# Optimization experiments

Measured on AMD Instinct MI355X. Metric: run time of the kernel, lower is better.

Reference implementation:

```python
import jax, jax.numpy as jnp
import numpy as np

H = 4  # head_num
K_CONV = 1  # convolution_num


def mhsa_mean(x, Wq, Wk, Wv, Wo):
    # x: [..., L, d]; standard multi-head self-attention followed by mean over L
    d = x.shape[-1]
    hd = d // H
    q = (x @ Wq).reshape(x.shape[:-1] + (H, hd))
    k = (x @ Wk).reshape(x.shape[:-1] + (H, hd))
    v = (x @ Wv).reshape(x.shape[:-1] + (H, hd))
    scores = jnp.einsum('...lhd,...mhd->...hlm', q, k) / jnp.sqrt(jnp.asarray(hd, x.dtype))
    attn = jax.nn.softmax(scores, axis=-1)
    o = jnp.einsum('...hlm,...mhd->...lhd', attn, v).reshape(x.shape) @ Wo
    return o.mean(axis=-2)


def setup_inputs() -> dict:
    key = jax.random.key(0)
    ks = jax.random.split(key, 18)
    WORD, QUERY, ENT, REV = 50000, 50000, 100000, 100000
    DW, DE = 64, 64
    LQ, LR, E, B = 8, 8, 2000000, 1024
    W_word = jax.random.normal(ks[0], (WORD, DW), jnp.float32) * 0.02
    W_word = W_word.at[0].set(0.0)  # padding_idx=0
    W_query = jax.random.normal(ks[1], (QUERY, DE), jnp.float32) * 0.02
    W_entity = jax.random.normal(ks[2], (ENT, DE), jnp.float32) * 0.02
    Wq = jax.random.normal(ks[3], (DW, DW), jnp.float32) * 0.05
    Wk = jax.random.normal(ks[4], (DW, DW), jnp.float32) * 0.05
    Wv = jax.random.normal(ks[5], (DW, DW), jnp.float32) * 0.05
    Wo = jax.random.normal(ks[6], (DW, DW), jnp.float32) * 0.05
    query_word_ids = jax.random.randint(ks[7], (QUERY, LQ), 0, WORD)
    review_word_ids = jax.random.randint(ks[8], (REV, LR), 0, WORD)
    profile_dst = jax.random.randint(ks[9], (REV,), 0, ENT)
    p_src = jax.random.randint(ks[10], (E,), 0, ENT)
    p_dst = jax.random.randint(ks[11], (E,), 0, ENT)
    p_qid = jax.random.randint(ks[12], (E,), 0, QUERY)
    users = jax.random.randint(ks[13], (B,), 0, ENT)
    items = jax.random.randint(ks[14], (B,), 0, ENT)
    negs = jax.random.randint(ks[15], (B,), 0, ENT)
    query_words = jax.random.randint(ks[16], (B, LQ), 0, WORD)
    return {'W_word': W_word, 'W_query': W_query, 'W_entity': W_entity,
            'Wq': Wq, 'Wk': Wk, 'Wv': Wv, 'Wo': Wo,
            'query_word_ids': query_word_ids, 'review_word_ids': review_word_ids,
            'profile_dst': profile_dst, 'p_src': p_src, 'p_dst': p_dst, 'p_qid': p_qid,
            'users': users, 'items': items, 'negs': negs, 'query_words': query_words}


def reference(W_word, W_query, W_entity, Wq, Wk, Wv, Wo,
              query_word_ids, review_word_ids, profile_dst, p_src, p_dst, p_qid,
              users, items, negs, query_words):
    N = W_entity.shape[0]
    DE = W_query.shape[1]
    # --- doc embeddings via MHSA+mean over composing words ---
    h_query = mhsa_mean(W_word[query_word_ids], Wq, Wk, Wv, Wo)    # [Q, DW]
    h_review = mhsa_mean(W_word[review_word_ids], Wq, Wk, Wv, Wo)  # [R, DW]
    # --- profiles: sum reviews into entities, degree-normalize ---
    deg_p = jnp.maximum(jax.ops.segment_sum(jnp.ones(profile_dst.shape[0], jnp.float32), profile_dst, num_segments=N), 1.0)
    ent_h = jax.ops.segment_sum(h_review, profile_dst, num_segments=N) / deg_p[:, None]
    q_e0 = jnp.concatenate([W_query, h_query], axis=-1)   # [Q, D]
    e_k = jnp.concatenate([W_entity, ent_h], axis=-1)     # e_0 [N, D]
    # --- interaction degrees: out-deg(purchased) + out-deg(purchased_by) ---
    ones_e = jnp.ones(p_src.shape[0], jnp.float32)
    deg_i = jax.ops.segment_sum(ones_e, p_src, num_segments=N) + jax.ops.segment_sum(ones_e, p_dst, num_segments=N)
    inv_sqrt = 1.0 / jnp.sqrt(jnp.maximum(deg_i, 1.0))    # [N]
    q_edge = q_e0[p_qid]                                   # [E, D]
    e_acc = e_k
    for _ in range(K_CONV):
        # purchased: m = src.e_k + q_e0[q_id] / sqrt(deg_i[src]); sum to dst
        msg = e_k[p_src] + q_edge * inv_sqrt[p_src][:, None]
        agg = jax.ops.segment_sum(msg, p_dst, num_segments=N)
        # purchased_by (reverse edges): m = e_k[src]/sqrt(deg_i[src]); sum to dst
        agg = agg + jax.ops.segment_sum(e_k[p_dst] * inv_sqrt[p_dst][:, None], p_src, num_segments=N)
        e_k = agg * inv_sqrt[:, None]
        e_acc = e_acc + e_k
    e = e_acc / (K_CONV + 1)                               # [N, D]
    # --- batch forward (train mode) ---
    qb = mhsa_mean(W_word[query_words], Wq, Wk, Wv, Wo)    # [B, DW]
    qb = jnp.concatenate([jnp.zeros((qb.shape[0], DE), qb.dtype), qb], axis=-1)
    personalized = e[users] + qb
    return personalized, e[items], e[negs]
```

## Files before the change

kernel.cpp:

```cpp
#include <hip/hip_runtime.h>

typedef unsigned int uint;
typedef unsigned short ushort;

typedef __bf16 bf16x8 __attribute__((ext_vector_type(8)));
typedef float f32x4 __attribute__((ext_vector_type(4)));
union U8 { uint4 u4; uint w[4]; bf16x8 b; };

__device__ __forceinline__ float bf2f(ushort u) {
    return __uint_as_float(((uint)u) << 16);
}
__device__ __forceinline__ float2 bfp2f(uint u) {
    float2 r;
    r.x = __uint_as_float(u << 16);
    r.y = __uint_as_float(u & 0xffff0000u);
    return r;
}
__device__ __forceinline__ ushort f2bf(float f) {
    uint u = __float_as_uint(f);
    return (ushort)((u + 0x7fffu + ((u >> 16) & 1u)) >> 16);
}

__global__ void mark_kernel(const int* __restrict__ users,
                            const int* __restrict__ items,
                            const int* __restrict__ negs,
                            int* __restrict__ mapid, int* __restrict__ mcnt,
                            int B) {
    int t = blockIdx.x * blockDim.x + threadIdx.x;
    if (t >= 3 * B) return;
    int n = t < B ? users[t] : (t < 2 * B ? items[t - B] : negs[t - 2 * B]);
    int old = atomicCAS(&mapid[n], -1, -2);
    if (old == -1) mapid[n] = atomicAdd(mcnt, 1);
}

__global__ void pre_kernel(const float* __restrict__ W_word,
                           const float* __restrict__ Wq,
                           const float* __restrict__ Wk,
                           const float* __restrict__ Wv,
                           const float* __restrict__ Wo,
                           ushort* __restrict__ Pq, ushort* __restrict__ Pk,
                           ushort* __restrict__ Vt,
                           const float* __restrict__ W_query,
                           const float* __restrict__ W_entity,
                           ushort* __restrict__ qe0b, ushort* __restrict__ e0b,
                           const int* __restrict__ p_src,
                           const int* __restrict__ p_dst,
                           const int* __restrict__ profile_dst,
                           const int* __restrict__ mapid,
                           int* __restrict__ degc, int* __restrict__ degp,
                           int* __restrict__ deg2,
                           int WORD, int Qn, int N, int E, int R,
                           int nc_blk, int npj_blk, int ncq_blk, int nce_blk) {
    int bid = blockIdx.x;
    int g = bid >> 3, j = bid & 7;
    if ((g & 3) == 3) {
        int idx = (g >> 2) * 8 + j;
        if (idx >= nc_blk) return;
        int t = idx * 256 + threadIdx.x;
        if (t < E) {
            int s = p_src[t], d = p_dst[t];
            atomicAdd(&degc[s], 1);
            atomicAdd(&degc[d], 1);
            int md = mapid[d]; if (md >= 0) atomicAdd(&deg2[md], 1);
            int ms = mapid[s]; if (ms >= 0) atomicAdd(&deg2[ms], 1);
        }
        if (t < R) atomicAdd(&degp[profile_dst[t]], 1);
        return;
    }
    int idx = ((g >> 2) * 3 + (g & 3)) * 8 + j;
    if (idx < npj_blk) {
        int wid  = idx * 4 + (threadIdx.x >> 6);
        int lane = threadIdx.x & 63;
        if (wid >= WORD) return;
        float x = W_word[(size_t)wid * 64 + lane];
        float aq = 0.f, ak = 0.f, av = 0.f;
#pragma unroll
        for (int i = 0; i < 64; i++) {
            float xi = __shfl(x, i, 64);
            aq = fmaf(xi, Wq[i * 64 + lane], aq);
            ak = fmaf(xi, Wk[i * 64 + lane], ak);
            av = fmaf(xi, Wv[i * 64 + lane], av);
        }
        size_t o = (size_t)wid * 64 + lane;
        Pq[o] = f2bf(aq); Pk[o] = f2bf(ak);
        float vt[4] = {0.f, 0.f, 0.f, 0.f};
#pragma unroll
        for (int i = 0; i < 64; i++) {
            float vi = __shfl(av, i, 64);
            vt[i >> 4] = fmaf(vi, Wo[i * 64 + lane], vt[i >> 4]);
        }
#pragma unroll
        for (int h = 0; h < 4; h++)
            Vt[((size_t)wid * 4 + h) * 64 + lane] = f2bf(vt[h]);
    } else if (idx < npj_blk + ncq_blk) {
        int t = (idx - npj_blk) * 256 + threadIdx.x;
        if (t >= Qn * 16) return;
        int r = t >> 4, c = (t & 15) * 4;
        const float4 v = *(const float4*)(W_query + (size_t)r * 64 + c);
        ushort4 o;
        o.x = f2bf(v.x); o.y = f2bf(v.y); o.z = f2bf(v.z); o.w = f2bf(v.w);
        *(ushort4*)(qe0b + (size_t)r * 128 + c) = o;
    } else if (idx < npj_blk + ncq_blk + nce_blk) {
        int t = (idx - npj_blk - ncq_blk) * 256 + threadIdx.x;
        if (t >= N * 16) return;
        int r = t >> 4, c = (t & 15) * 4;
        const float4 v = *(const float4*)(W_entity + (size_t)r * 64 + c);
        ushort4 o;
        o.x = f2bf(v.x); o.y = f2bf(v.y); o.z = f2bf(v.z); o.w = f2bf(v.w);
        *(ushort4*)(e0b + (size_t)r * 128 + c) = o;
    }
}

__global__ void scan_sum(const int* __restrict__ degp, int* __restrict__ csum,
                         int N) {
    __shared__ int red[4];
    int chunk = blockIdx.x, t = threadIdx.x;
    int base = chunk * 1024;
    int v = 0;
#pragma unroll
    for (int k = 0; k < 4; k++) {
        int idx = base + t * 4 + k;
        if (idx < N) v += degp[idx];
    }
#pragma unroll
    for (int o = 32; o; o >>= 1) v += __shfl_down(v, o, 64);
    if ((t & 63) == 0) red[t >> 6] = v;
    __syncthreads();
    if (t == 0) csum[chunk] = red[0] + red[1] + red[2] + red[3];
}

__global__ void scan_mid(int* __restrict__ csum, int nchunk,
                         const int* __restrict__ deg2,
                         int* __restrict__ offs2, int* __restrict__ cursor2,
                         int nb2) {
    __shared__ int lds[256];
    int t = threadIdx.x;
    int v = (t < nchunk) ? csum[t] : 0;
    lds[t] = v;
    __syncthreads();
    for (int o = 1; o < 256; o <<= 1) {
        int u = (t >= o) ? lds[t - o] : 0;
        __syncthreads();
        lds[t] += u;
        __syncthreads();
    }
    if (t < nchunk) csum[t] = lds[t] - v;
    __syncthreads();
    int k2 = nb2 >> 8;
    int s = 0;
    for (int k = 0; k < k2; k++) s += deg2[t * k2 + k];
    lds[t] = s;
    __syncthreads();
    for (int o = 1; o < 256; o <<= 1) {
        int u = (t >= o) ? lds[t - o] : 0;
        __syncthreads();
        lds[t] += u;
        __syncthreads();
    }
    int tb = lds[t] - s;
    for (int k = 0; k < k2; k++) {
        int dv = deg2[t * k2 + k];
        offs2[t * k2 + k] = tb;
        cursor2[t * k2 + k] = tb;
        tb += dv;
    }
    if (t == 255) offs2[nb2] = tb;
}

__global__ void scan_chunk(const int* __restrict__ degp,
                           const int* __restrict__ csum,
                           const int* __restrict__ degc,
                           int* __restrict__ offs_r, int* __restrict__ cursor_r,
                           float* __restrict__ inv, int N) {
    __shared__ int lds[256];
    int chunk = blockIdx.x, t = threadIdx.x;
    int base = chunk * 1024 + t * 4;
    int v0 = (base + 0 < N) ? degp[base + 0] : 0;
    int v1 = (base + 1 < N) ? degp[base + 1] : 0;
    int v2 = (base + 2 < N) ? degp[base + 2] : 0;
    int v3 = (base + 3 < N) ? degp[base + 3] : 0;
    if (base + 0 < N) inv[base + 0] = 1.0f / sqrtf((float)max(degc[base + 0], 1));
    if (base + 1 < N) inv[base + 1] = 1.0f / sqrtf((float)max(degc[base + 1], 1));
    if (base + 2 < N) inv[base + 2] = 1.0f / sqrtf((float)max(degc[base + 2], 1));
    if (base + 3 < N) inv[base + 3] = 1.0f / sqrtf((float)max(degc[base + 3], 1));
    int s = v0 + v1 + v2 + v3;
    lds[t] = s;
    __syncthreads();
    for (int o = 1; o < 256; o <<= 1) {
        int u = (t >= o) ? lds[t - o] : 0;
        __syncthreads();
        lds[t] += u;
        __syncthreads();
    }
    int tb = lds[t] - s + csum[chunk];
    int vv[4] = {v0, v1, v2, v3};
#pragma unroll
    for (int k = 0; k < 4; k++) {
        int idx = base + k;
        if (idx < N) {
            offs_r[idx] = tb; cursor_r[idx] = tb; tb += vv[k];
            if (idx == N - 1) offs_r[N] = tb;
        }
    }
}

__device__ __forceinline__ void mhsa_pair(const ushort* __restrict__ Pq,
                                          const ushort* __restrict__ Pk,
                                          const ushort* __restrict__ Vt,
                                          const int* __restrict__ ids,
                                          int wid2, int lane, int mode,
                                          ushort* __restrict__ outb,
                                          float* __restrict__ outf) {
    const int l15 = lane & 15;
    const int gi  = lane >> 4;
    const int hs  = gi >> 1;
    const int dbase = (gi & 1) * 8;
    const int* idr = ids + (size_t)wid2 * 16;
    const bool valid = hs == (l15 >> 3);

    const int myid = idr[l15];
    int vid[8];
#pragma unroll
    for (int i = 0; i < 8; i++) vid[i] = idr[dbase + i];

    uint pk4[4][2];
    const f32x4 zero4 = {0.f, 0.f, 0.f, 0.f};
#pragma unroll
    for (int h = 0; h < 4; h++) {
        U8 a, b;
        if (valid) {
            a.u4 = *(const uint4*)(Pk + (size_t)myid * 64 + h * 16 + dbase);
            b.u4 = *(const uint4*)(Pq + (size_t)myid * 64 + h * 16 + dbase);
        } else {
            a.u4 = make_uint4(0, 0, 0, 0);
            b.u4 = make_uint4(0, 0, 0, 0);
        }
        f32x4 d = __builtin_amdgcn_mfma_f32_16x16x32_bf16(a.b, b.b, zero4, 0, 0, 0);
        float s0 = d[0] * 0.25f, s1 = d[1] * 0.25f;
        float s2 = d[2] * 0.25f, s3 = d[3] * 0.25f;
        if (!valid) { s0 = s1 = s2 = s3 = -1e30f; }
        float mx = fmaxf(fmaxf(s0, s1), fmaxf(s2, s3));
        mx = fmaxf(mx, __shfl_xor(mx, 16, 64));
        mx = fmaxf(mx, __shfl_xor(mx, 32, 64));
        float x0 = __expf(s0 - mx), x1 = __expf(s1 - mx);
        float x2 = __expf(s2 - mx), x3 = __expf(s3 - mx);
        float sm = x0 + x1 + x2 + x3;
        sm += __shfl_xor(sm, 16, 64);
        sm += __shfl_xor(sm, 32, 64);
        float f = 0.125f / sm;
        uint w0 = (uint)f2bf(x0 * f) | ((uint)f2bf(x1 * f) << 16);
        uint w1 = (uint)f2bf(x2 * f) | ((uint)f2bf(x3 * f) << 16);
        pk4[h][0] = valid ? w0 : 0u;
        pk4[h][1] = valid ? w1 : 0u;
    }

    const int srcA = l15 + (gi & 1) * 32;
    const int srcB = srcA + 16;
    uint aw[2][4];
#pragma unroll
    for (int P = 0; P < 2; P++) {
        uint r00 = (uint)__shfl((int)pk4[2 * P][0], srcA, 64);
        uint r01 = (uint)__shfl((int)pk4[2 * P][1], srcA, 64);
        uint r02 = (uint)__shfl((int)pk4[2 * P][0], srcB, 64);
        uint r03 = (uint)__shfl((int)pk4[2 * P][1], srcB, 64);
        uint r10 = (uint)__shfl((int)pk4[2 * P + 1][0], srcA, 64);
        uint r11 = (uint)__shfl((int)pk4[2 * P + 1][1], srcA, 64);
        uint r12 = (uint)__shfl((int)pk4[2 * P + 1][0], srcB, 64);
        uint r13 = (uint)__shfl((int)pk4[2 * P + 1][1], srcB, 64);
        aw[P][0] = hs ? r10 : r00;
        aw[P][1] = hs ? r11 : r01;
        aw[P][2] = hs ? r12 : r02;
        aw[P][3] = hs ? r13 : r03;
    }

    size_t vb[8];
#pragma unroll
    for (int i = 0; i < 8; i++) vb[i] = (size_t)vid[i] * 256;
#pragma unroll
    for (int t = 0; t < 4; t++) {
        const int col = t * 16 + l15;
        f32x4 acc = zero4;
#pragma unroll
        for (int P = 0; P < 2; P++) {
            const int h = 2 * P + hs;
            uint e[8];
#pragma unroll
            for (int i = 0; i < 8; i++) e[i] = Vt[vb[i] + h * 64 + col];
            U8 bv;
            bv.w[0] = e[0] | (e[1] << 16);
            bv.w[1] = e[2] | (e[3] << 16);
            bv.w[2] = e[4] | (e[5] << 16);
            bv.w[3] = e[6] | (e[7] << 16);
            U8 av_;
            av_.w[0] = aw[P][0]; av_.w[1] = aw[P][1];
            av_.w[2] = aw[P][2]; av_.w[3] = aw[P][3];
            acc = __builtin_amdgcn_mfma_f32_16x16x32_bf16(av_.b, bv.b, acc, 0, 0, 0);
        }
        float s = acc[0] + acc[1] + acc[2] + acc[3];
        s += __shfl_xor(s, 16, 64);
        if ((gi & 1) == 0) {
            int row = wid2 * 2 + hs;
            if (mode == 0)      outb[(size_t)row * 128 + 64 + col] = f2bf(s);
            else if (mode == 1) outb[(size_t)row * 64 + col] = f2bf(s);
            else                outf[(size_t)row * 64 + col] = s;
        }
    }
}

__global__ void mega_kernel(const ushort* __restrict__ Pq,
                            const ushort* __restrict__ Pk,
                            const ushort* __restrict__ Vt,
                            const int* __restrict__ query_word_ids,
                            const int* __restrict__ review_word_ids,
                            const int* __restrict__ query_words,
                            ushort* __restrict__ qe0b,
                            ushort* __restrict__ hrev,
                            float* __restrict__ qb,
                            const int* __restrict__ p_src,
                            const int* __restrict__ p_dst,
                            const int* __restrict__ p_qid,
                            const int* __restrict__ profile_dst,
                            const int* __restrict__ mapid,
                            int* __restrict__ cursor2, int2* __restrict__ list2,
                            int* __restrict__ cursor_r, int* __restrict__ rmsg,
                            int Qn, int R, int B, int E,
                            int nr_blk, int nq_blk, int nb_blk,
                            int np_blk, int nv_blk) {
    int bid = blockIdx.x;
    int g = bid >> 3, j = bid & 7;
    if ((g & 3) == 3) {
        int idx = (g >> 2) * 8 + j;
        if (idx < np_blk) {
            int base = idx * 512 + threadIdx.x;
#pragma unroll
            for (int k = 0; k < 2; k++) {
                int e = base + k * 256;
                if (e < E) {
                    int s = p_src[e], d = p_dst[e];
                    int md = mapid[d], ms = mapid[s];
                    if (md >= 0)
                        list2[atomicAdd(&cursor2[md], 1)] = make_int2(s, p_qid[e]);
                    if (ms >= 0)
                        list2[atomicAdd(&cursor2[ms], 1)] = make_int2(d, -1);
                }
            }
        } else if (idx < np_blk + nv_blk) {
            int r = (idx - np_blk) * 256 + threadIdx.x;
            if (r >= R) return;
            rmsg[atomicAdd(&cursor_r[profile_dst[r]], 1)] = r;
        }
        return;
    }
    int idx = ((g >> 2) * 3 + (g & 3)) * 8 + j;
    int lane = threadIdx.x & 63;
    int w = threadIdx.x >> 6;
    if (idx < nr_blk) {
        int wid2 = idx * 4 + w;
        if (wid2 < (R >> 1))
            mhsa_pair(Pq, Pk, Vt, review_word_ids, wid2, lane, 1, hrev, nullptr);
    } else if (idx < nr_blk + nq_blk) {
        int wid2 = (idx - nr_blk) * 4 + w;
        if (wid2 < (Qn >> 1))
            mhsa_pair(Pq, Pk, Vt, query_word_ids, wid2, lane, 0, qe0b, nullptr);
    } else if (idx < nr_blk + nq_blk + nb_blk) {
        int wid2 = (idx - nr_blk - nq_blk) * 4 + w;
        if (wid2 < (B >> 1))
            mhsa_pair(Pq, Pk, Vt, query_words, wid2, lane, 2, nullptr, qb);
    }
}

__global__ void entity_gather(const ushort* __restrict__ hrev,
                              const int* __restrict__ offs_r,
                              const int* __restrict__ rmsg,
                              ushort* __restrict__ e0b, int N) {
    int g = (blockIdx.x * blockDim.x + threadIdx.x) >> 4;
    int c = (threadIdx.x & 15) * 4;
    if (g >= N) return;
    int beg = offs_r[g], end = offs_r[g + 1];
    float a0 = 0.f, a1 = 0.f, a2 = 0.f, a3 = 0.f;
    for (int m = beg; m < end; m++) {
        int r = rmsg[m];
        ushort4 v = *(const ushort4*)(hrev + (size_t)r * 64 + c);
        a0 += bf2f(v.x); a1 += bf2f(v.y); a2 += bf2f(v.z); a3 += bf2f(v.w);
    }
    float s = 1.0f / (float)max(end - beg, 1);
    ushort4 o;
    o.x = f2bf(a0 * s); o.y = f2bf(a1 * s); o.z = f2bf(a2 * s); o.w = f2bf(a3 * s);
    *(ushort4*)(e0b + (size_t)g * 128 + 64 + c) = o;
}

__global__ void gather_out(const ushort* __restrict__ e0b,
                           const ushort* __restrict__ qe0b,
                           const float* __restrict__ inv,
                           const int* __restrict__ mapid,
                           const int* __restrict__ offs2,
                           const int2* __restrict__ list2,
                           const float* __restrict__ qb,
                           const int* __restrict__ users,
                           const int* __restrict__ items,
                           const int* __restrict__ negs,
                           float* __restrict__ out, int B) {
    int slot = (blockIdx.x * blockDim.x + threadIdx.x) >> 4;
    int c = (threadIdx.x & 15) * 8;
    if (slot >= 3 * B) return;
    int which = slot / B, b = slot - which * B;
    int node = which == 0 ? users[b] : (which == 1 ? items[b] : negs[b]);
    int m = mapid[node];
    int beg = offs2[m], end = offs2[m + 1];
    float a0 = 0.f, a1 = 0.f, a2 = 0.f, a3 = 0.f;
    float a4 = 0.f, a5 = 0.f, a6 = 0.f, a7 = 0.f;
    for (int i = beg; i < end; i++) {
        int2 mm = list2[i];
        float w = inv[mm.x];
        const uint4 ev = *(const uint4*)(e0b + (size_t)mm.x * 128 + c);
        if (mm.y >= 0) {
            const uint4 qv = *(const uint4*)(qe0b + (size_t)mm.y * 128 + c);
            float2 e, q;
            e = bfp2f(ev.x); q = bfp2f(qv.x); a0 += fmaf(q.x, w, e.x); a1 += fmaf(q.y, w, e.y);
            e = bfp2f(ev.y); q = bfp2f(qv.y); a2 += fmaf(q.x, w, e.x); a3 += fmaf(q.y, w, e.y);
            e = bfp2f(ev.z); q = bfp2f(qv.z); a4 += fmaf(q.x, w, e.x); a5 += fmaf(q.y, w, e.y);
            e = bfp2f(ev.w); q = bfp2f(qv.w); a6 += fmaf(q.x, w, e.x); a7 += fmaf(q.y, w, e.y);
        } else {
            float2 e;
            e = bfp2f(ev.x); a0 = fmaf(e.x, w, a0); a1 = fmaf(e.y, w, a1);
            e = bfp2f(ev.y); a2 = fmaf(e.x, w, a2); a3 = fmaf(e.y, w, a3);
            e = bfp2f(ev.z); a4 = fmaf(e.x, w, a4); a5 = fmaf(e.y, w, a5);
            e = bfp2f(ev.w); a6 = fmaf(e.x, w, a6); a7 = fmaf(e.y, w, a7);
        }
    }
    float wn = inv[node];
    const uint4 sv = *(const uint4*)(e0b + (size_t)node * 128 + c);
    float2 e0v;
    float r0, r1, r2, r3, r4, r5, r6, r7;
    e0v = bfp2f(sv.x); r0 = 0.5f * fmaf(a0, wn, e0v.x); r1 = 0.5f * fmaf(a1, wn, e0v.y);
    e0v = bfp2f(sv.y); r2 = 0.5f * fmaf(a2, wn, e0v.x); r3 = 0.5f * fmaf(a3, wn, e0v.y);
    e0v = bfp2f(sv.z); r4 = 0.5f * fmaf(a4, wn, e0v.x); r5 = 0.5f * fmaf(a5, wn, e0v.y);
    e0v = bfp2f(sv.w); r6 = 0.5f * fmaf(a6, wn, e0v.x); r7 = 0.5f * fmaf(a7, wn, e0v.y);
    if (which == 0 && c >= 64) {
        const float4 q0 = *(const float4*)(qb + (size_t)b * 64 + (c - 64));
        const float4 q1 = *(const float4*)(qb + (size_t)b * 64 + (c - 60));
        r0 += q0.x; r1 += q0.y; r2 += q0.z; r3 += q0.w;
        r4 += q1.x; r5 += q1.y; r6 += q1.z; r7 += q1.w;
    }
    float* dst = out + (size_t)which * B * 128 + (size_t)b * 128 + c;
    float4 w0; w0.x = r0; w0.y = r1; w0.z = r2; w0.w = r3;
    float4 w1; w1.x = r4; w1.y = r5; w1.z = r6; w1.w = r7;
    *(float4*)dst = w0;
    *(float4*)(dst + 4) = w1;
}

extern "C" void kernel_launch(void* const* d_in, const int* in_sizes, int n_in,
                              void* d_out, int out_size, void* d_ws, size_t ws_size,
                              hipStream_t stream) {
    const float* W_word   = (const float*)d_in[0];
    const float* W_query  = (const float*)d_in[1];
    const float* W_entity = (const float*)d_in[2];
    const float* Wq       = (const float*)d_in[3];
    const float* Wk       = (const float*)d_in[4];
    const float* Wv       = (const float*)d_in[5];
    const float* Wo       = (const float*)d_in[6];
    const int* query_word_ids  = (const int*)d_in[7];
    const int* review_word_ids = (const int*)d_in[8];
    const int* profile_dst     = (const int*)d_in[9];
    const int* p_src  = (const int*)d_in[10];
    const int* p_dst  = (const int*)d_in[11];
    const int* p_qid  = (const int*)d_in[12];
    const int* users  = (const int*)d_in[13];
    const int* items  = (const int*)d_in[14];
    const int* negs   = (const int*)d_in[15];
    const int* query_words = (const int*)d_in[16];

    const int WORD = in_sizes[0] / 64;
    const int Qn   = in_sizes[1] / 64;
    const int N    = in_sizes[2] / 64;
    const int R    = in_sizes[8] / 8;
    const int E    = in_sizes[10];
    const int B    = in_sizes[13];

    const int NB2 = ((3 * B + 255) / 256) * 256;

    ushort* e0b  = (ushort*)d_ws;
    ushort* qe0b = e0b + (size_t)N * 128;
    ushort* Pq   = qe0b + (size_t)Qn * 128;
    ushort* Pk   = Pq + (size_t)WORD * 64;
    ushort* Vt   = Pk + (size_t)WORD * 64;
    ushort* hrev = Vt + (size_t)WORD * 256;
    float*  qb   = (float*)(hrev + (size_t)R * 64);
    float*  inv  = qb + (size_t)B * 64;
    int* degc     = (int*)(inv + N);
    int* degp     = degc + N;
    int* deg2     = degp + N;
    int* mcnt     = deg2 + NB2;
    int* mapid    = mcnt + 4;
    int* offs_r   = mapid + N;
    int* cursor_r = offs_r + N + 2;
    int* csum     = cursor_r + N;
    int* offs2    = csum + 256;
    int* cursor2  = offs2 + NB2 + 1;
    int* rmsg     = cursor2 + NB2;
    int2* list2   = (int2*)(rmsg + R);

    const int nchunk = (N + 1023) / 1024;

    hipMemsetAsync(degc, 0, (2 * (size_t)N + NB2 + 4) * sizeof(int), stream);
    hipMemsetAsync(mapid, 0xFF, (size_t)N * sizeof(int), stream);

    mark_kernel<<<(3 * B + 255) / 256, 256, 0, stream>>>(users, items, negs,
                                                         mapid, mcnt, B);

    {
        int nc_blk  = (E + 255) / 256;
        int npj_blk = (WORD + 3) / 4;
        int ncq_blk = (Qn * 16 + 255) / 256;
        int nce_blk = (N * 16 + 255) / 256;
        int mh_fam  = npj_blk + ncq_blk + nce_blk;
        int T = max(4 * nc_blk, (mh_fam * 4 + 2) / 3);
        T = ((T + 31) / 32) * 32;
        pre_kernel<<<T, 256, 0, stream>>>(W_word, Wq, Wk, Wv, Wo, Pq, Pk, Vt,
                                          W_query, W_entity, qe0b, e0b,
                                          p_src, p_dst, profile_dst, mapid,
                                          degc, degp, deg2,
                                          WORD, Qn, N, E, R,
                                          nc_blk, npj_blk, ncq_blk, nce_blk);
    }

    scan_sum<<<nchunk, 256, 0, stream>>>(degp, csum, N);
    scan_mid<<<1, 256, 0, stream>>>(csum, nchunk, deg2, offs2, cursor2, NB2);
    scan_chunk<<<nchunk, 256, 0, stream>>>(degp, csum, degc, offs_r, cursor_r, inv, N);

    {
        int nr_blk = (R / 2 + 3) / 4;
        int nq_blk = (Qn / 2 + 3) / 4;
        int nb_blk = (B / 2 + 3) / 4;
        int np_blk = (E + 511) / 512;
        int nv_blk = (R + 255) / 256;
        int sc = np_blk + nv_blk;
        int mh = nr_blk + nq_blk + nb_blk;
        int T = max(4 * sc, (mh * 4 + 2) / 3);
        T = ((T + 31) / 32) * 32;
        mega_kernel<<<T, 256, 0, stream>>>(Pq, Pk, Vt,
                                           query_word_ids, review_word_ids, query_words,
                                           qe0b, hrev, qb,
                                           p_src, p_dst, p_qid, profile_dst, mapid,
                                           cursor2, list2, cursor_r, rmsg,
                                           Qn, R, B, E,
                                           nr_blk, nq_blk, nb_blk, np_blk, nv_blk);
    }

    entity_gather<<<(N * 16 + 255) / 256, 256, 0, stream>>>(hrev, offs_r, rmsg, e0b, N);

    gather_out<<<(3 * B * 16 + 255) / 256, 256, 0, stream>>>(e0b, qe0b, inv,
                                                             mapid, offs2, list2,
                                                             qb, users, items, negs,
                                                             (float*)d_out, B);
}
```

Measured before the change: 509.9 us.

## Use MFMA for word projections and defer Wo projection to a post-aggregation pass

The per-word Q/K/V projections now run on bf16 MFMA over 16-word tiles using pre-swizzled weights, replacing the scalar shuffle-FMA loop. The Wo output projection is no longer folded into per-head V tables (Vt, four times larger); instead plain Pv is gathered in attention, and Wo is applied afterwards on the mean-aggregated entity, query and batch rows in a new wo_kernel, relying on the projection being linear. The degree-count branch also processes two edges per thread. This cuts the work and size of the V table gathers and speeds up the projection, but adds two extra kernel launches and extra bf16 intermediate buffers, with rounding at different points.

```diff
diff --git a/kernel.cpp b/kernel.cpp
--- a/kernel.cpp
+++ b/kernel.cpp
@@ -19,6 +19,14 @@
 __device__ __forceinline__ ushort f2bf(float f) {
     uint u = __float_as_uint(f);
     return (ushort)((u + 0x7fffu + ((u >> 16) & 1u)) >> 16);
+}
+__device__ __forceinline__ uint4 pack8(float4 a, float4 b) {
+    uint4 u;
+    u.x = (uint)f2bf(a.x) | ((uint)f2bf(a.y) << 16);
+    u.y = (uint)f2bf(a.z) | ((uint)f2bf(a.w) << 16);
+    u.z = (uint)f2bf(b.x) | ((uint)f2bf(b.y) << 16);
+    u.w = (uint)f2bf(b.z) | ((uint)f2bf(b.w) << 16);
+    return u;
 }
 
 __global__ void mark_kernel(const int* __restrict__ users,
@@ -33,13 +41,35 @@
     if (old == -1) mapid[n] = atomicAdd(mcnt, 1);
 }
 
+__global__ void wswz_kernel(const float* __restrict__ Wq,
+                            const float* __restrict__ Wk,
+                            const float* __restrict__ Wv,
+                            const float* __restrict__ Wo,
+                            ushort* __restrict__ wsw, ushort* __restrict__ wswo) {
+    int e = blockIdx.x * 256 + threadIdx.x;
+    if (e < 12288) {
+        int f = e >> 9, r = e & 511;
+        int lane = r >> 3, i = r & 7;
+        int ct = f >> 1, kh = f & 1;
+        int k = kh * 32 + (lane >> 4) * 8 + i;
+        int col = (ct & 3) * 16 + (lane & 15);
+        const float* W = ct < 4 ? Wq : (ct < 8 ? Wk : Wv);
+        wsw[f * 512 + lane * 8 + i] = f2bf(W[k * 64 + col]);
+    } else if (e < 16384) {
+        int e2 = e - 12288;
+        int f = e2 >> 9, r = e2 & 511;
+        int lane = r >> 3, i = r & 7;
+        int ct = f >> 1, kh = f & 1;
+        int k = kh * 32 + (lane >> 4) * 8 + i;
+        int col = ct * 16 + (lane & 15);
+        wswo[f * 512 + lane * 8 + i] = f2bf(Wo[k * 64 + col]);
+    }
+}
+
 __global__ void pre_kernel(const float* __restrict__ W_word,
-                           const float* __restrict__ Wq,
-                           const float* __restrict__ Wk,
-                           const float* __restrict__ Wv,
-                           const float* __restrict__ Wo,
+                           const ushort* __restrict__ wsw,
                            ushort* __restrict__ Pq, ushort* __restrict__ Pk,
-                           ushort* __restrict__ Vt,
+                           ushort* __restrict__ Pv,
                            const float* __restrict__ W_query,
                            const float* __restrict__ W_entity,
                            ushort* __restrict__ qe0b, ushort* __restrict__ e0b,
@@ -56,42 +86,44 @@
     if ((g & 3) == 3) {
         int idx = (g >> 2) * 8 + j;
         if (idx >= nc_blk) return;
-        int t = idx * 256 + threadIdx.x;
-        if (t < E) {
-            int s = p_src[t], d = p_dst[t];
-            atomicAdd(&degc[s], 1);
-            atomicAdd(&degc[d], 1);
-            int md = mapid[d]; if (md >= 0) atomicAdd(&deg2[md], 1);
-            int ms = mapid[s]; if (ms >= 0) atomicAdd(&deg2[ms], 1);
-        }
-        if (t < R) atomicAdd(&degp[profile_dst[t]], 1);
+        int base = idx * 512 + threadIdx.x;
+#pragma unroll
+        for (int k = 0; k < 2; k++) {
+            int t = base + k * 256;
+            if (t < E) {
+                int s = p_src[t], d = p_dst[t];
+                atomicAdd(&degc[s], 1);
+                atomicAdd(&degc[d], 1);
+                int md = mapid[d]; if (md >= 0) atomicAdd(&deg2[md], 1);
+                int ms = mapid[s]; if (ms >= 0) atomicAdd(&deg2[ms], 1);
+            }
+            if (t < R) atomicAdd(&degp[profile_dst[t]], 1);
+        }
         return;
     }
     int idx = ((g >> 2) * 3 + (g & 3)) * 8 + j;
     if (idx < npj_blk) {
-        int wid  = idx * 4 + (threadIdx.x >> 6);
-        int lane = threadIdx.x & 63;
-        if (wid >= WORD) return;
-        float x = W_word[(size_t)wid * 64 + lane];
-        float aq = 0.f, ak = 0.f, av = 0.f;
-#pragma unroll
-        for (int i = 0; i < 64; i++) {
-            float xi = __shfl(x, i, 64);
-            aq = fmaf(xi, Wq[i * 64 + lane], aq);
-            ak = fmaf(xi, Wk[i * 64 + lane], ak);
-            av = fmaf(xi, Wv[i * 64 + lane], av);
-        }
-        size_t o = (size_t)wid * 64 + lane;
-        Pq[o] = f2bf(aq); Pk[o] = f2bf(ak);
-        float vt[4] = {0.f, 0.f, 0.f, 0.f};
-#pragma unroll
-        for (int i = 0; i < 64; i++) {
-            float vi = __shfl(av, i, 64);
-            vt[i >> 4] = fmaf(vi, Wo[i * 64 + lane], vt[i >> 4]);
-        }
-#pragma unroll
-        for (int h = 0; h < 4; h++)
-            Vt[((size_t)wid * 4 + h) * 64 + lane] = f2bf(vt[h]);
+        int tile = idx * 4 + (threadIdx.x >> 6);
+        if (tile * 16 >= WORD) return;
+        int lane = threadIdx.x & 63, l15 = lane & 15, gi = lane >> 4;
+        const float* xr = W_word + ((size_t)tile * 16 + l15) * 64 + gi * 8;
+        U8 a0, a1;
+        a0.u4 = pack8(*(const float4*)(xr), *(const float4*)(xr + 4));
+        a1.u4 = pack8(*(const float4*)(xr + 32), *(const float4*)(xr + 36));
+        const f32x4 zero4 = {0.f, 0.f, 0.f, 0.f};
+#pragma unroll
+        for (int ct = 0; ct < 12; ct++) {
+            U8 b0, b1;
+            b0.u4 = *(const uint4*)(wsw + (ct * 2 + 0) * 512 + lane * 8);
+            b1.u4 = *(const uint4*)(wsw + (ct * 2 + 1) * 512 + lane * 8);
+            f32x4 acc = __builtin_amdgcn_mfma_f32_16x16x32_bf16(a0.b, b0.b, zero4, 0, 0, 0);
+            acc = __builtin_amdgcn_mfma_f32_16x16x32_bf16(a1.b, b1.b, acc, 0, 0, 0);
+            ushort* dst = ct < 4 ? Pq : (ct < 8 ? Pk : Pv);
+            int col = (ct & 3) * 16 + l15;
+#pragma unroll
+            for (int r = 0; r < 4; r++)
+                dst[((size_t)tile * 16 + gi * 4 + r) * 64 + col] = f2bf(acc[r]);
+        }
     } else if (idx < npj_blk + ncq_blk) {
         int t = (idx - npj_blk) * 256 + threadIdx.x;
         if (t >= Qn * 16) return;
@@ -206,11 +238,10 @@
 
 __device__ __forceinline__ void mhsa_pair(const ushort* __restrict__ Pq,
                                           const ushort* __restrict__ Pk,
-                                          const ushort* __restrict__ Vt,
+                                          const ushort* __restrict__ Pv,
                                           const int* __restrict__ ids,
-                                          int wid2, int lane, int mode,
-                                          ushort* __restrict__ outb,
-                                          float* __restrict__ outf) {
+                                          int wid2, int lane,
+                                          ushort* __restrict__ outb) {
     const int l15 = lane & 15;
     const int gi  = lane >> 4;
     const int hs  = gi >> 1;
@@ -256,66 +287,47 @@
 
     const int srcA = l15 + (gi & 1) * 32;
     const int srcB = srcA + 16;
-    uint aw[2][4];
-#pragma unroll
-    for (int P = 0; P < 2; P++) {
-        uint r00 = (uint)__shfl((int)pk4[2 * P][0], srcA, 64);
-        uint r01 = (uint)__shfl((int)pk4[2 * P][1], srcA, 64);
-        uint r02 = (uint)__shfl((int)pk4[2 * P][0], srcB, 64);
-        uint r03 = (uint)__shfl((int)pk4[2 * P][1], srcB, 64);
-        uint r10 = (uint)__shfl((int)pk4[2 * P + 1][0], srcA, 64);
-        uint r11 = (uint)__shfl((int)pk4[2 * P + 1][1], srcA, 64);
-        uint r12 = (uint)__shfl((int)pk4[2 * P + 1][0], srcB, 64);
-        uint r13 = (uint)__shfl((int)pk4[2 * P + 1][1], srcB, 64);
-        aw[P][0] = hs ? r10 : r00;
-        aw[P][1] = hs ? r11 : r01;
-        aw[P][2] = hs ? r12 : r02;
-        aw[P][3] = hs ? r13 : r03;
-    }
-
+    const bool hi = gi >= 2;
     size_t vb[8];
 #pragma unroll
-    for (int i = 0; i < 8; i++) vb[i] = (size_t)vid[i] * 256;
+    for (int i = 0; i < 8; i++) vb[i] = (size_t)vid[i] * 64;
 #pragma unroll
     for (int t = 0; t < 4; t++) {
-        const int col = t * 16 + l15;
-        f32x4 acc = zero4;
-#pragma unroll
-        for (int P = 0; P < 2; P++) {
-            const int h = 2 * P + hs;
-            uint e[8];
-#pragma unroll
-            for (int i = 0; i < 8; i++) e[i] = Vt[vb[i] + h * 64 + col];
-            U8 bv;
-            bv.w[0] = e[0] | (e[1] << 16);
-            bv.w[1] = e[2] | (e[3] << 16);
-            bv.w[2] = e[4] | (e[5] << 16);
-            bv.w[3] = e[6] | (e[7] << 16);
-            U8 av_;
-            av_.w[0] = aw[P][0]; av_.w[1] = aw[P][1];
-            av_.w[2] = aw[P][2]; av_.w[3] = aw[P][3];
-            acc = __builtin_amdgcn_mfma_f32_16x16x32_bf16(av_.b, bv.b, acc, 0, 0, 0);
-        }
+        uint aw0 = (uint)__shfl((int)pk4[t][0], srcA, 64);
+        uint aw1 = (uint)__shfl((int)pk4[t][1], srcA, 64);
+        uint aw2 = (uint)__shfl((int)pk4[t][0], srcB, 64);
+        uint aw3 = (uint)__shfl((int)pk4[t][1], srcB, 64);
+        U8 av_;
+        av_.w[0] = hi ? 0u : aw0; av_.w[1] = hi ? 0u : aw1;
+        av_.w[2] = hi ? 0u : aw2; av_.w[3] = hi ? 0u : aw3;
+        uint e[8];
+#pragma unroll
+        for (int i = 0; i < 8; i++)
+            e[i] = hi ? 0u : (uint)Pv[vb[i] + t * 16 + l15];
+        U8 bv;
+        bv.w[0] = e[0] | (e[1] << 16);
+        bv.w[1] = e[2] | (e[3] << 16);
+        bv.w[2] = e[4] | (e[5] << 16);
+        bv.w[3] = e[6] | (e[7] << 16);
+        f32x4 acc = __builtin_amdgcn_mfma_f32_16x16x32_bf16(av_.b, bv.b, zero4, 0, 0, 0);
         float s = acc[0] + acc[1] + acc[2] + acc[3];
         s += __shfl_xor(s, 16, 64);
         if ((gi & 1) == 0) {
             int row = wid2 * 2 + hs;
-            if (mode == 0)      outb[(size_t)row * 128 + 64 + col] = f2bf(s);
-            else if (mode == 1) outb[(size_t)row * 64 + col] = f2bf(s);
-            else                outf[(size_t)row * 64 + col] = s;
+            outb[(size_t)row * 64 + t * 16 + l15] = f2bf(s);
         }
     }
 }
 
 __global__ void mega_kernel(const ushort* __restrict__ Pq,
                             const ushort* __restrict__ Pk,
-                            const ushort* __restrict__ Vt,
+                            const ushort* __restrict__ Pv,
                             const int* __restrict__ query_word_ids,
                             const int* __restrict__ review_word_ids,
                             const int* __restrict__ query_words,
-                            ushort* __restrict__ qe0b,
+                            ushort* __restrict__ hqom,
                             ushort* __restrict__ hrev,
-                            float* __restrict__ qb,
+                            ushort* __restrict__ omb,
                             const int* __restrict__ p_src,
                             const int* __restrict__ p_dst,
                             const int* __restrict__ p_qid,
@@ -357,22 +369,22 @@
     if (idx < nr_blk) {
         int wid2 = idx * 4 + w;
         if (wid2 < (R >> 1))
-            mhsa_pair(Pq, Pk, Vt, review_word_ids, wid2, lane, 1, hrev, nullptr);
+            mhsa_pair(Pq, Pk, Pv, review_word_ids, wid2, lane, hrev);
     } else if (idx < nr_blk + nq_blk) {
         int wid2 = (idx - nr_blk) * 4 + w;
         if (wid2 < (Qn >> 1))
-            mhsa_pair(Pq, Pk, Vt, query_word_ids, wid2, lane, 0, qe0b, nullptr);
+            mhsa_pair(Pq, Pk, Pv, query_word_ids, wid2, lane, hqom);
     } else if (idx < nr_blk + nq_blk + nb_blk) {
         int wid2 = (idx - nr_blk - nq_blk) * 4 + w;
         if (wid2 < (B >> 1))
-            mhsa_pair(Pq, Pk, Vt, query_words, wid2, lane, 2, nullptr, qb);
+            mhsa_pair(Pq, Pk, Pv, query_words, wid2, lane, omb);
     }
 }
 
 __global__ void entity_gather(const ushort* __restrict__ hrev,
                               const int* __restrict__ offs_r,
                               const int* __restrict__ rmsg,
-                              ushort* __restrict__ e0b, int N) {
+                              ushort* __restrict__ eom, int N) {
     int g = (blockIdx.x * blockDim.x + threadIdx.x) >> 4;
     int c = (threadIdx.x & 15) * 4;
     if (g >= N) return;
@@ -386,7 +398,46 @@
     float s = 1.0f / (float)max(end - beg, 1);
     ushort4 o;
     o.x = f2bf(a0 * s); o.y = f2bf(a1 * s); o.z = f2bf(a2 * s); o.w = f2bf(a3 * s);
-    *(ushort4*)(e0b + (size_t)g * 128 + 64 + c) = o;
+    *(ushort4*)(eom + (size_t)g * 64 + c) = o;
+}
+
+__global__ void wo_kernel(const ushort* __restrict__ eom,
+                          const ushort* __restrict__ hqom,
+                          const ushort* __restrict__ omb,
+                          const ushort* __restrict__ wswo,
+                          ushort* __restrict__ e0b, ushort* __restrict__ qe0b,
+                          float* __restrict__ qb, int N, int Qn, int B) {
+    int tile = blockIdx.x * 4 + (threadIdx.x >> 6);
+    int ntile = (N + Qn + B) >> 4;
+    if (tile >= ntile) return;
+    int lane = threadIdx.x & 63, l15 = lane & 15, gi = lane >> 4;
+    int row0 = tile << 4;
+    int region; int rb;
+    const ushort* src;
+    if (row0 < N)            { region = 0; rb = row0;            src = eom; }
+    else if (row0 < N + Qn)  { region = 1; rb = row0 - N;        src = hqom; }
+    else                     { region = 2; rb = row0 - N - Qn;   src = omb; }
+    const ushort* sr = src + ((size_t)rb + l15) * 64;
+    U8 a0, a1;
+    a0.u4 = *(const uint4*)(sr + gi * 8);
+    a1.u4 = *(const uint4*)(sr + 32 + gi * 8);
+    const f32x4 zero4 = {0.f, 0.f, 0.f, 0.f};
+#pragma unroll
+    for (int ct = 0; ct < 4; ct++) {
+        U8 b0, b1;
+        b0.u4 = *(const uint4*)(wswo + (ct * 2 + 0) * 512 + lane * 8);
+        b1.u4 = *(const uint4*)(wswo + (ct * 2 + 1) * 512 + lane * 8);
+        f32x4 acc = __builtin_amdgcn_mfma_f32_16x16x32_bf16(a0.b, b0.b, zero4, 0, 0, 0);
+        acc = __builtin_amdgcn_mfma_f32_16x16x32_bf16(a1.b, b1.b, acc, 0, 0, 0);
+        int col = ct * 16 + l15;
+#pragma unroll
+        for (int r = 0; r < 4; r++) {
+            int row = rb + gi * 4 + r;
+            if (region == 0)      e0b[(size_t)row * 128 + 64 + col] = f2bf(acc[r]);
+            else if (region == 1) qe0b[(size_t)row * 128 + 64 + col] = f2bf(acc[r]);
+            else                  qb[(size_t)row * 64 + col] = acc[r];
+        }
+    }
 }
 
 __global__ void gather_out(const ushort* __restrict__ e0b,
@@ -483,9 +534,14 @@
     ushort* qe0b = e0b + (size_t)N * 128;
     ushort* Pq   = qe0b + (size_t)Qn * 128;
     ushort* Pk   = Pq + (size_t)WORD * 64;
-    ushort* Vt   = Pk + (size_t)WORD * 64;
-    ushort* hrev = Vt + (size_t)WORD * 256;
-    float*  qb   = (float*)(hrev + (size_t)R * 64);
+    ushort* Pv   = Pk + (size_t)WORD * 64;
+    ushort* hrev = Pv + (size_t)WORD * 64;
+    ushort* hqom = hrev + (size_t)R * 64;
+    ushort* omb  = hqom + (size_t)Qn * 64;
+    ushort* eom  = omb + (size_t)B * 64;
+    ushort* wsw  = eom + (size_t)N * 64;
+    ushort* wswo = wsw + 12288;
+    float*  qb   = (float*)(wswo + 4096);
     float*  inv  = qb + (size_t)B * 64;
     int* degc     = (int*)(inv + N);
     int* degp     = degc + N;
@@ -496,7 +552,7 @@
     int* cursor_r = offs_r + N + 2;
     int* csum     = cursor_r + N;
     int* offs2    = csum + 256;
-    int* cursor2  = offs2 + NB2 + 1;
+    int* cursor2  = offs2 + NB2 + 2;
     int* rmsg     = cursor2 + NB2;
     int2* list2   = (int2*)(rmsg + R);
 
@@ -507,16 +563,17 @@
 
     mark_kernel<<<(3 * B + 255) / 256, 256, 0, stream>>>(users, items, negs,
                                                          mapid, mcnt, B);
+    wswz_kernel<<<64, 256, 0, stream>>>(Wq, Wk, Wv, Wo, wsw, wswo);
 
     {
-        int nc_blk  = (E + 255) / 256;
-        int npj_blk = (WORD + 3) / 4;
+        int nc_blk  = (E + 511) / 512;
+        int npj_blk = (WORD / 16 + 3) / 4;
         int ncq_blk = (Qn * 16 + 255) / 256;
         int nce_blk = (N * 16 + 255) / 256;
         int mh_fam  = npj_blk + ncq_blk + nce_blk;
         int T = max(4 * nc_blk, (mh_fam * 4 + 2) / 3);
         T = ((T + 31) / 32) * 32;
-        pre_kernel<<<T, 256, 0, stream>>>(W_word, Wq, Wk, Wv, Wo, Pq, Pk, Vt,
+        pre_kernel<<<T, 256, 0, stream>>>(W_word, wsw, Pq, Pk, Pv,
                                           W_query, W_entity, qe0b, e0b,
                                           p_src, p_dst, profile_dst, mapid,
                                           degc, degp, deg2,
@@ -538,16 +595,22 @@
         int mh = nr_blk + nq_blk + nb_blk;
         int T = max(4 * sc, (mh * 4 + 2) / 3);
         T = ((T + 31) / 32) * 32;
-        mega_kernel<<<T, 256, 0, stream>>>(Pq, Pk, Vt,
+        mega_kernel<<<T, 256, 0, stream>>>(Pq, Pk, Pv,
                                            query_word_ids, review_word_ids, query_words,
-                                           qe0b, hrev, qb,
+                                           hqom, hrev, omb,
                                            p_src, p_dst, p_qid, profile_dst, mapid,
                                            cursor2, list2, cursor_r, rmsg,
                                            Qn, R, B, E,
                                            nr_blk, nq_blk, nb_blk, np_blk, nv_blk);
     }
 
-    entity_gather<<<(N * 16 + 255) / 256, 256, 0, stream>>>(hrev, offs_r, rmsg, e0b, N);
+    entity_gather<<<(N * 16 + 255) / 256, 256, 0, stream>>>(hrev, offs_r, rmsg, eom, N);
+
+    {
+        int ntile = (N + Qn + B) / 16;
+        wo_kernel<<<(ntile + 3) / 4, 256, 0, stream>>>(eom, hqom, omb, wswo,
+                                                       e0b, qe0b, qb, N, Qn, B);
+    }
 
     gather_out<<<(3 * B * 16 + 255) / 256, 256, 0, stream>>>(e0b, qe0b, inv,
                                                              mapid, offs2, list2,
```

Result: faster. 440.2 us (-13.7%).
